# Performance work log

Hardware: AMD Instinct MI355X
Metric: run time of the kernel (lower is better)

Reference implementation:

```python
import jax, jax.numpy as jnp
import numpy as np
import math

THETA = 10000.0

def apply_rope(x):
    # x: [B, H, S, D] with D even; interleaved even/odd rotation
    B, H, S, D = x.shape
    dim_half = D // 2
    freq_idx = jnp.arange(dim_half, dtype=jnp.float32)
    inv_freq = jnp.exp(-math.log(THETA) * freq_idx * 2.0 / D)  # [D/2]
    pos = jnp.arange(S, dtype=jnp.float32)
    angles = pos[:, None] * inv_freq[None, :]      # [S, D/2]
    cos = jnp.cos(angles)[None, None]              # [1,1,S,D/2]
    sin = jnp.sin(angles)[None, None]
    x_even = x[..., ::2]
    x_odd = x[..., 1::2]
    r_even = x_even * cos - x_odd * sin
    r_odd = x_odd * cos + x_even * sin
    return jnp.stack([r_even, r_odd], axis=-1).reshape(B, H, S, D)

def setup_inputs() -> dict:
    key = jax.random.key(0)
    ks = jax.random.split(key, 5)
    B, S, E = 2, 2048, 1024
    std = 0.02
    inp = {
        "hidden_states": jax.random.normal(ks[0], (B, S, E), dtype=jnp.float32),
        "Wq": jax.random.normal(ks[1], (E, E), dtype=jnp.float32) * std,
        "bq": jnp.zeros((E,), dtype=jnp.float32),
        "Wk": jax.random.normal(ks[2], (E, E), dtype=jnp.float32) * std,
        "bk": jnp.zeros((E,), dtype=jnp.float32),
        "Wv": jax.random.normal(ks[3], (E, E), dtype=jnp.float32) * std,
        "bv": jnp.zeros((E,), dtype=jnp.float32),
        "Wo": jax.random.normal(ks[4], (E, E), dtype=jnp.float32) * std,
        "bo": jnp.zeros((E,), dtype=jnp.float32),
    }
    return inp

def reference(hidden_states, Wq, bq, Wk, bk, Wv, bv, Wo, bo):
    NUM_HEADS = 16
    B, S, E = hidden_states.shape
    D = E // NUM_HEADS
    scale = 1.0 / math.sqrt(D)

    def proj(W, b):
        # torch Linear: x @ W.T + b; then [B,S,H,D] -> [B,H,S,D]
        y = hidden_states @ W.T + b
        return y.reshape(B, S, NUM_HEADS, D).transpose(0, 2, 1, 3)

    q = apply_rope(proj(Wq, bq))
    k = apply_rope(proj(Wk, bk))
    v = proj(Wv, bv)

    scores = jnp.einsum("bhqd,bhkd->bhqk", q, k) * scale
    attn = jax.nn.softmax(scores, axis=-1)
    out = jnp.einsum("bhqk,bhkd->bhqd", attn, v)  # [B,H,S,D]
    out = out.transpose(0, 2, 1, 3).reshape(B, S, E)
    return out @ Wo.T + bo  # dropout: eval mode (identity)
```

## Files before the change

kernel.cpp:

```cpp
#include <hip/hip_runtime.h>
#include <hip/hip_bf16.h>
#include <math.h>

#define B_ 2
#define S_ 2048
#define E_ 1024
#define H_ 16
#define D_ 64
#define M_ (B_*S_)
#define PT 32

typedef short bf16x8 __attribute__((ext_vector_type(8)));
typedef float f32x4 __attribute__((ext_vector_type(4)));
typedef unsigned short u16x4 __attribute__((ext_vector_type(4)));

#define SCLQ 0.18033688011112042f

__device__ __forceinline__ unsigned short f2bf(float f) {
    unsigned int u = __builtin_bit_cast(unsigned int, f);
    u += 0x7FFFu + ((u >> 16) & 1u);
    return (unsigned short)(u >> 16);
}
__device__ __forceinline__ unsigned int pk2bf(float a, float b) {
    __hip_bfloat162 h = __float22bfloat162_rn(make_float2(a, b));
    unsigned int u;
    __builtin_memcpy(&u, &h, 4);
    return u;
}
__device__ __forceinline__ f32x4 mfma16(bf16x8 a, bf16x8 b, f32x4 c) {
    return __builtin_amdgcn_mfma_f32_16x16x32_bf16(a, b, c, 0, 0, 0);
}
__device__ __forceinline__ bf16x8 cvt8(const float* p) {
    f32x4 lo = *(const f32x4*)p;
    f32x4 hi = *(const f32x4*)(p + 4);
    unsigned int pk[4];
    pk[0] = pk2bf(lo[0], lo[1]);
    pk[1] = pk2bf(lo[2], lo[3]);
    pk[2] = pk2bf(hi[0], hi[1]);
    pk[3] = pk2bf(hi[2], hi[3]);
    bf16x8 r;
    __builtin_memcpy(&r, pk, 16);
    return r;
}
__device__ __forceinline__ void g2l16(const unsigned short* g, unsigned short* l) {
    __builtin_amdgcn_global_load_lds(
        (const __attribute__((address_space(1))) unsigned int*)(const void*)g,
        (__attribute__((address_space(3))) unsigned int*)(void*)l,
        16, 0, 0);
}

__global__ __launch_bounds__(256) void cvt_kernel(
    const float* __restrict__ X,  const float* __restrict__ Wq,
    const float* __restrict__ Wk, const float* __restrict__ Wv,
    const float* __restrict__ Wo,
    unsigned short* __restrict__ Xb, unsigned short* __restrict__ Wb,
    float* __restrict__ tab)
{
    const int y = blockIdx.y;
    if (y == 5) {
        unsigned int i = blockIdx.x * 256 + threadIdx.x;
        if (i < 32 * 2048) {
            int f = i >> 11, s = i & 2047;
            const float C = -0.41524101186091903f;
            const float INV2PI = 0.15915494309189535f;
            float inv_rev = exp2f(C * (float)f) * INV2PI;
            float rev = (float)s * inv_rev;
            float fr = rev - rintf(rev);
            tab[i]           = __builtin_amdgcn_cosf(fr);
            tab[65536 + i]   = __builtin_amdgcn_sinf(fr);
        }
        return;
    }
    const float* src = (y == 0) ? X : (y == 1) ? Wq : (y == 2) ? Wk : (y == 3) ? Wv : Wo;
    unsigned short* dst = (y == 0) ? Xb : Wb + (size_t)(y - 1) * (E_ * E_);
    const size_t n = (y == 0) ? (size_t)M_ * E_ : (size_t)E_ * E_;
    size_t i = ((size_t)blockIdx.x * 256 + threadIdx.x) * 8;
    if (i < n) *(bf16x8*)(dst + i) = cvt8(src + i);
}

__global__ __launch_bounds__(256, 4) void qkv_rope_bf(
    const unsigned short* __restrict__ Xb, const unsigned short* __restrict__ Wb,
    const float* __restrict__ bq, const float* __restrict__ bk,
    const float* __restrict__ bv, const float* __restrict__ tab,
    unsigned short* __restrict__ Qo, unsigned short* __restrict__ Ko,
    unsigned short* __restrict__ Vo)
{
    __shared__ __align__(16) unsigned char lds_raw[128 * 132 * 2];
    unsigned short* As = (unsigned short*)lds_raw;
    unsigned short* Bs = (unsigned short*)(lds_raw + 8192);
    unsigned short* Cs = (unsigned short*)lds_raw;

    const int t = threadIdx.x;
    const int w = t >> 6, lane = t & 63, quad = lane >> 4, l16 = lane & 15;
    const int wr = (w >> 1) * 64, wc = (w & 1) * 64;
    const int n0 = blockIdx.x * 128, m0 = blockIdx.y * 128;
    const int z = blockIdx.z;
    const unsigned short* W = Wb + (size_t)z * (E_ * E_);
    const float* bias = (z == 0) ? bq : (z == 1) ? bk : bv;

    const int r4 = t >> 2, c8 = (t & 3) * 8;
    const unsigned short* Ag = Xb + (size_t)(m0 + r4) * E_ + c8;
    const unsigned short* Bg = W  + (size_t)(n0 + r4) * E_ + c8;

    f32x4 zero = {0.f, 0.f, 0.f, 0.f};
    f32x4 acc[4][4];
#pragma unroll
    for (int i = 0; i < 4; i++)
#pragma unroll
        for (int j = 0; j < 4; j++) acc[i][j] = zero;

    for (int kt = 0; kt < E_; kt += 32) {
        __syncthreads();
        g2l16(Ag + kt,           &As[t * 8]);
        g2l16(Ag + 64 * E_ + kt, &As[t * 8 + 2048]);
        g2l16(Bg + kt,           &Bs[t * 8]);
        g2l16(Bg + 64 * E_ + kt, &Bs[t * 8 + 2048]);
        __syncthreads();
        bf16x8 af[4], bfr[4];
#pragma unroll
        for (int i = 0; i < 4; i++)
            af[i] = *(const bf16x8*)&As[(wr + i * 16 + l16) * 32 + quad * 8];
#pragma unroll
        for (int j = 0; j < 4; j++)
            bfr[j] = *(const bf16x8*)&Bs[(wc + j * 16 + l16) * 32 + quad * 8];
#pragma unroll
        for (int i = 0; i < 4; i++)
#pragma unroll
            for (int j = 0; j < 4; j++)
                acc[i][j] = mfma16(af[i], bfr[j], acc[i][j]);
    }

    __syncthreads();
    const int seg = quad;
    if (z < 2) {
        const float qscale = (z == 0) ? SCLQ : 1.0f;
#pragma unroll
        for (int j = 0; j < 4; j++) {
            int n_local = wc + j * 16 + l16;
            int n = n0 + n_local;
            int d = n & 63, f = d >> 1;
            float bvv = bias[n];
            float sgn = (d & 1) ? 1.f : -1.f;
            const float* ct = tab + f * 2048;
            const float* st_ = tab + 65536 + f * 2048;
#pragma unroll
            for (int i = 0; i < 4; i++) {
                int mb = wr + i * 16 + quad * 4;
                int sb = (m0 + mb) & (S_ - 1);
                f32x4 cs4 = *(const f32x4*)&ct[sb];
                f32x4 sn4 = *(const f32x4*)&st_[sb];
#pragma unroll
                for (int r = 0; r < 4; r++) {
                    float val = acc[i][j][r] + bvv;
                    float oth = __shfl_xor(val, 1);
                    Cs[(mb + r) * 132 + n_local] =
                        f2bf((val * cs4[r] + sgn * oth * sn4[r]) * qscale);
                }
            }
        }
        __syncthreads();
        unsigned short* Out = (z == 0) ? Qo : Ko;
        const int btok = m0 >> 11;
        const int half = seg & 1;
#pragma unroll
        for (int it = 0; it < 16; it++) {
            int m_local = it * 8 + w * 2 + (seg >> 1);
            int s = (m0 + m_local) & (S_ - 1);
            int h = (n0 + half * 64) >> 6;
            u16x4 v = *(const u16x4*)&Cs[m_local * 132 + half * 64 + l16 * 4];
            *(u16x4*)&Out[(((size_t)btok * H_ + h) * S_ + s) * D_ + l16 * 4] = v;
        }
    } else {
#pragma unroll
        for (int j = 0; j < 4; j++) {
            int n_local = wc + j * 16 + l16;
            float bvv = bias[n0 + n_local];
#pragma unroll
            for (int i = 0; i < 4; i++) {
                int mb = wr + i * 16 + quad * 4;
#pragma unroll
                for (int r = 0; r < 4; r++)
                    Cs[n_local * 132 + mb + r] = f2bf(acc[i][j][r] + bvv);
            }
        }
        __syncthreads();
        const int btok = m0 >> 11;
        const int s0 = m0 & (S_ - 1);
        const int half = seg & 1;
#pragma unroll
        for (int it = 0; it < 16; it++) {
            int n_local = it * 8 + w * 2 + (seg >> 1);
            int n = n0 + n_local;
            int h = n >> 6, d = n & 63;
            u16x4 v = *(const u16x4*)&Cs[n_local * 132 + half * 64 + l16 * 4];
            *(u16x4*)&Vo[(((size_t)btok * H_ + h) * D_ + d) * S_ + s0 + half * 64 + l16 * 4] = v;
        }
    }
}

__global__ __launch_bounds__(512, 3) void attn_direct(
    const unsigned short* __restrict__ Q, const unsigned short* __restrict__ K,
    const unsigned short* __restrict__ Vt, unsigned short* __restrict__ ctx)
{
    __shared__ unsigned short KsD[2][64 * 64];
    __shared__ unsigned short VsD[2][64 * 64];
    __shared__ unsigned short Ps[8][16 * 72];
    const int t = threadIdx.x;
    const int w = t >> 6, lane = t & 63, quad = lane >> 4, l16 = lane & 15;
    const int bh = blockIdx.y;
    const int q0 = blockIdx.x * 128 + w * 16;

    const unsigned short* Qg = Q + ((size_t)bh * S_ + q0) * D_;
    bf16x8 qf[2];
#pragma unroll
    for (int ks = 0; ks < 2; ks++)
        qf[ks] = *(const bf16x8*)(Qg + (size_t)l16 * 64 + ks * 32 + quad * 8);

    bf16x8 ones;
#pragma unroll
    for (int e = 0; e < 8; e++) ones[e] = (short)0x3F80;

    f32x4 zero = {0.f, 0.f, 0.f, 0.f};
    f32x4 acc_o[4];
    f32x4 acc_l = zero;
#pragma unroll
    for (int j = 0; j < 4; j++) acc_o[j] = zero;

    const int tt = t & 255, ksel = t >> 8;
    const int sr = tt >> 2;
    const int sc = ((tt & 3) ^ ((tt >> 3) & 3)) * 8;
    const unsigned short* KgL = K  + (size_t)bh * S_ * D_ + (size_t)sr * 64 + ksel * 32 + sc;
    const unsigned short* VgL = Vt + (size_t)bh * D_ * S_ + (size_t)sr * S_ + ksel * 32 + sc;

    const int sl = (quad ^ ((l16 >> 1) & 3)) * 8;

    g2l16(KgL, &KsD[0][t * 8]);
    g2l16(VgL, &VsD[0][t * 8]);
    __syncthreads();

    int p = 0;
    for (int kt = 0; kt < S_; kt += 64) {
        if (kt + 64 < S_) {
            g2l16(KgL + (size_t)(kt + 64) * 64, &KsD[1 - p][t * 8]);
            g2l16(VgL + (kt + 64),              &VsD[1 - p][t * 8]);
        }

        f32x4 sc4[4];
#pragma unroll
        for (int j = 0; j < 4; j++) sc4[j] = zero;
#pragma unroll
        for (int ks = 0; ks < 2; ks++) {
#pragma unroll
            for (int j = 0; j < 4; j++) {
                bf16x8 kf = *(const bf16x8*)&KsD[p][ks * 2048 + (j * 16 + l16) * 32 + sl];
                sc4[j] = mfma16(qf[ks], kf, sc4[j]);
            }
        }
#pragma unroll
        for (int j = 0; j < 4; j++)
#pragma unroll
            for (int r = 0; r < 4; r += 2) {
                float pa = __builtin_amdgcn_exp2f(sc4[j][r]);
                float pb = __builtin_amdgcn_exp2f(sc4[j][r + 1]);
                unsigned int u = pk2bf(pa, pb);
                Ps[w][(quad * 4 + r)     * 72 + j * 16 + l16] = (unsigned short)u;
                Ps[w][(quad * 4 + r + 1) * 72 + j * 16 + l16] = (unsigned short)(u >> 16);
            }
#pragma unroll
        for (int ks = 0; ks < 2; ks++) {
            bf16x8 pf = *(const bf16x8*)&Ps[w][l16 * 72 + ks * 32 + quad * 8];
#pragma unroll
            for (int jd = 0; jd < 4; jd++) {
                bf16x8 vf = *(const bf16x8*)&VsD[p][ks * 2048 + (jd * 16 + l16) * 32 + sl];
                acc_o[jd] = mfma16(pf, vf, acc_o[jd]);
            }
            acc_l = mfma16(pf, ones, acc_l);
        }

        __syncthreads();
        p ^= 1;
    }

    const int b = bh >> 4, h = bh & 15;
    f32x4 rl;
#pragma unroll
    for (int r = 0; r < 4; r++) rl[r] = 1.0f / acc_l[r];
#pragma unroll
    for (int jd = 0; jd < 4; jd++)
#pragma unroll
        for (int r = 0; r < 4; r++) {
            int qrow = q0 + quad * 4 + r;
            int col = h * 64 + jd * 16 + l16;
            ctx[((size_t)b * S_ + qrow) * E_ + col] = f2bf(acc_o[jd][r] * rl[r]);
        }
}

__global__ __launch_bounds__(256, 4) void out_bf(
    const unsigned short* __restrict__ Cx, const unsigned short* __restrict__ Wob,
    const float* __restrict__ bo, float* __restrict__ out)
{
    __shared__ unsigned short As[128 * 32];
    __shared__ unsigned short Bs[64 * 32];
    const int t = threadIdx.x;
    const int w = t >> 6, lane = t & 63, quad = lane >> 4, l16 = lane & 15;
    const int m0 = blockIdx.y * 128, n0 = blockIdx.x * 64;
    const int wr = w * 32;
    const int r4 = t >> 2, c8 = (t & 3) * 8;
    const unsigned short* Ag = Cx  + (size_t)(m0 + r4) * E_ + c8;
    const unsigned short* Bg = Wob + (size_t)(n0 + r4) * E_ + c8;

    f32x4 zero = {0.f, 0.f, 0.f, 0.f};
    f32x4 acc[2][4];
#pragma unroll
    for (int i = 0; i < 2; i++)
#pragma unroll
        for (int j = 0; j < 4; j++) acc[i][j] = zero;

    for (int kt = 0; kt < E_; kt += 32) {
        __syncthreads();
        g2l16(Ag + kt,           &As[t * 8]);
        g2l16(Ag + 64 * E_ + kt, &As[t * 8 + 2048]);
        g2l16(Bg + kt,           &Bs[t * 8]);
        __syncthreads();
        bf16x8 af[2], bfr[4];
#pragma unroll
        for (int i = 0; i < 2; i++)
            af[i] = *(const bf16x8*)&As[(wr + i * 16 + l16) * 32 + quad * 8];
#pragma unroll
        for (int j = 0; j < 4; j++)
            bfr[j] = *(const bf16x8*)&Bs[(j * 16 + l16) * 32 + quad * 8];
#pragma unroll
        for (int i = 0; i < 2; i++)
#pragma unroll
            for (int j = 0; j < 4; j++)
                acc[i][j] = mfma16(af[i], bfr[j], acc[i][j]);
    }

#pragma unroll
    for (int j = 0; j < 4; j++) {
        int n = n0 + j * 16 + l16;
        float bvv = bo[n];
#pragma unroll
        for (int i = 0; i < 2; i++) {
            int mrow = m0 + wr + i * 16 + quad * 4;
#pragma unroll
            for (int r = 0; r < 4; r++)
                out[(size_t)(mrow + r) * E_ + n] = acc[i][j][r] + bvv;
        }
    }
}

__global__ __launch_bounds__(256, 3) void qkv_rope_f32(
    const float* __restrict__ X,
    const float* __restrict__ Wq, const float* __restrict__ Wk,
    const float* __restrict__ Wv,
    const float* __restrict__ bq, const float* __restrict__ bk,
    const float* __restrict__ bv,
    unsigned short* __restrict__ Qo, unsigned short* __restrict__ Ko,
    unsigned short* __restrict__ Vo)
{
    __shared__ __align__(16) unsigned char lds_raw[128 * 132 * 2];
    unsigned short* As = (unsigned short*)lds_raw;
    unsigned short* Bs = (unsigned short*)(lds_raw + 8192);
    unsigned short* Cs = (unsigned short*)lds_raw;

    const int t = threadIdx.x;
    const int w = t >> 6, lane = t & 63, quad = lane >> 4, l16 = lane & 15;
    const int wr = (w >> 1) * 64, wc = (w & 1) * 64;
    const int n0 = blockIdx.x * 128, m0 = blockIdx.y * 128;
    const int z = blockIdx.z;
    const float* W    = (z == 0) ? Wq : (z == 1) ? Wk : Wv;
    const float* bias = (z == 0) ? bq : (z == 1) ? bk : bv;

    const int r4 = t >> 2, c8 = (t & 3) * 8;
    const int st = r4 * PT + c8;
    const float* Ag = X + (size_t)(m0 + r4) * E_ + c8;
    const float* Bg = W + (size_t)(n0 + r4) * E_ + c8;

    f32x4 zero = {0.f, 0.f, 0.f, 0.f};
    f32x4 acc[4][4];
#pragma unroll
    for (int i = 0; i < 4; i++)
#pragma unroll
        for (int j = 0; j < 4; j++) acc[i][j] = zero;

    for (int kt = 0; kt < E_; kt += 32) {
        bf16x8 a0 = cvt8(Ag + kt);
        bf16x8 a1 = cvt8(Ag + 64 * E_ + kt);
        bf16x8 b0 = cvt8(Bg + kt);
        bf16x8 b1 = cvt8(Bg + 64 * E_ + kt);
        __syncthreads();
        *(bf16x8*)&As[st]           = a0;
        *(bf16x8*)&As[st + 64 * PT] = a1;
        *(bf16x8*)&Bs[st]           = b0;
        *(bf16x8*)&Bs[st + 64 * PT] = b1;
        __syncthreads();
        bf16x8 af[4], bfr[4];
#pragma unroll
        for (int i = 0; i < 4; i++)
            af[i] = *(const bf16x8*)&As[(wr + i * 16 + l16) * PT + quad * 8];
#pragma unroll
        for (int j = 0; j < 4; j++)
            bfr[j] = *(const bf16x8*)&Bs[(wc + j * 16 + l16) * PT + quad * 8];
#pragma unroll
        for (int i = 0; i < 4; i++)
#pragma unroll
            for (int j = 0; j < 4; j++)
                acc[i][j] = mfma16(af[i], bfr[j], acc[i][j]);
    }

    __syncthreads();
    const int seg = quad;
    if (z < 2) {
        const float C = -0.41524101186091903f;
        const float INV2PI = 0.15915494309189535f;
        const float qscale = (z == 0) ? SCLQ : 1.0f;
#pragma unroll
        for (int j = 0; j < 4; j++) {
            int n_local = wc + j * 16 + l16;
            int n = n0 + n_local;
            int d = n & 63, f = d >> 1;
            float inv_rev = exp2f(C * (float)f) * INV2PI;
            float bvv = bias[n];
            float sgn = (d & 1) ? 1.f : -1.f;
#pragma unroll
            for (int i = 0; i < 4; i++) {
                int mb = wr + i * 16 + quad * 4;
#pragma unroll
                for (int r = 0; r < 4; r++) {
                    int m = m0 + mb + r;
                    int s = m & (S_ - 1);
                    float val = acc[i][j][r] + bvv;
                    float oth = __shfl_xor(val, 1);
                    float rev = (float)s * inv_rev;
                    float fr = rev - rintf(rev);
                    float sn = __builtin_amdgcn_sinf(fr);
                    float cs = __builtin_amdgcn_cosf(fr);
                    Cs[(mb + r) * 132 + n_local] =
                        f2bf((val * cs + sgn * oth * sn) * qscale);
                }
            }
        }
        __syncthreads();
        unsigned short* Out = (z == 0) ? Qo : Ko;
        const int btok = m0 >> 11;
        const int half = seg & 1;
#pragma unroll
        for (int it = 0; it < 16; it++) {
            int m_local = it * 8 + w * 2 + (seg >> 1);
            int s = (m0 + m_local) & (S_ - 1);
            int h = (n0 + half * 64) >> 6;
            u16x4 v = *(const u16x4*)&Cs[m_local * 132 + half * 64 + l16 * 4];
            *(u16x4*)&Out[(((size_t)btok * H_ + h) * S_ + s) * D_ + l16 * 4] = v;
        }
    } else {
#pragma unroll
        for (int j = 0; j < 4; j++) {
            int n_local = wc + j * 16 + l16;
            float bvv = bias[n0 + n_local];
#pragma unroll
            for (int i = 0; i < 4; i++) {
                int mb = wr + i * 16 + quad * 4;
#pragma unroll
                for (int r = 0; r < 4; r++)
                    Cs[n_local * 132 + mb + r] = f2bf(acc[i][j][r] + bvv);
            }
        }
        __syncthreads();
        const int btok = m0 >> 11;
        const int s0 = m0 & (S_ - 1);
        const int half = seg & 1;
#pragma unroll
        for (int it = 0; it < 16; it++) {
            int n_local = it * 8 + w * 2 + (seg >> 1);
            int n = n0 + n_local;
            int h = n >> 6, d = n & 63;
            u16x4 v = *(const u16x4*)&Cs[n_local * 132 + half * 64 + l16 * 4];
            *(u16x4*)&Vo[(((size_t)btok * H_ + h) * D_ + d) * S_ + s0 + half * 64 + l16 * 4] = v;
        }
    }
}

__global__ __launch_bounds__(256, 2) void out_f32(
    const unsigned short* __restrict__ Cx, const float* __restrict__ Wo,
    const float* __restrict__ bo, float* __restrict__ out)
{
    __shared__ unsigned short As[128 * PT];
    __shared__ unsigned short Bs[64 * PT];
    const int t = threadIdx.x;
    const int w = t >> 6, lane = t & 63, quad = lane >> 4, l16 = lane & 15;
    const int m0 = blockIdx.y * 128, n0 = blockIdx.x * 64;
    const int wr = w * 32;
    const int r4 = t >> 2, c8 = (t & 3) * 8;
    const int st = r4 * PT + c8;
    const unsigned short* Ag = Cx + (size_t)(m0 + r4) * E_ + c8;
    const float*          Bg = Wo + (size_t)(n0 + (r4 & 63)) * E_ + c8;

    f32x4 zero = {0.f, 0.f, 0.f, 0.f};
    f32x4 acc[2][4];
#pragma unroll
    for (int i = 0; i < 2; i++)
#pragma unroll
        for (int j = 0; j < 4; j++) acc[i][j] = zero;

    for (int kt = 0; kt < E_; kt += 32) {
        bf16x8 a0 = *(const bf16x8*)(Ag + kt);
        bf16x8 a1 = *(const bf16x8*)(Ag + 64 * E_ + kt);
        bf16x8 b0 = cvt8(Bg + kt);
        __syncthreads();
        *(bf16x8*)&As[st]           = a0;
        *(bf16x8*)&As[st + 64 * PT] = a1;
        *(bf16x8*)&Bs[st]           = b0;
        __syncthreads();
        bf16x8 af[2], bfr[4];
#pragma unroll
        for (int i = 0; i < 2; i++)
            af[i] = *(const bf16x8*)&As[(wr + i * 16 + l16) * PT + quad * 8];
#pragma unroll
        for (int j = 0; j < 4; j++)
            bfr[j] = *(const bf16x8*)&Bs[(j * 16 + l16) * PT + quad * 8];
#pragma unroll
        for (int i = 0; i < 2; i++)
#pragma unroll
            for (int j = 0; j < 4; j++)
                acc[i][j] = mfma16(af[i], bfr[j], acc[i][j]);
    }

#pragma unroll
    for (int j = 0; j < 4; j++) {
        int n = n0 + j * 16 + l16;
        float bvv = bo[n];
#pragma unroll
        for (int i = 0; i < 2; i++) {
            int mrow = m0 + wr + i * 16 + quad * 4;
#pragma unroll
            for (int r = 0; r < 4; r++)
                out[(size_t)(mrow + r) * E_ + n] = acc[i][j][r] + bvv;
        }
    }
}

extern "C" void kernel_launch(void* const* d_in, const int* in_sizes, int n_in,
                              void* d_out, int out_size, void* d_ws, size_t ws_size,
                              hipStream_t stream) {
    const float* X  = (const float*)d_in[0];
    const float* Wq = (const float*)d_in[1];
    const float* bq = (const float*)d_in[2];
    const float* Wk = (const float*)d_in[3];
    const float* bk = (const float*)d_in[4];
    const float* Wv = (const float*)d_in[5];
    const float* bv = (const float*)d_in[6];
    const float* Wo = (const float*)d_in[7];
    const float* bo = (const float*)d_in[8];
    float* outp = (float*)d_out;

    const size_t TN = (size_t)B_ * H_ * S_ * D_;
    const size_t need_f32 = 4 * TN * sizeof(unsigned short);
    const size_t need_bf  = 5 * TN * sizeof(unsigned short) + 2 * 65536 * sizeof(float);
    if (ws_size < need_f32) return;

    unsigned short* Qb = (unsigned short*)d_ws;
    unsigned short* Kb = Qb + TN;
    unsigned short* Vb = Kb + TN;

    if (ws_size >= need_bf) {
        unsigned short* Xb = Vb + TN;
        unsigned short* Wb = Xb + TN;
        float* tab = (float*)(Wb + 4 * (size_t)(E_ * E_));
        unsigned short* Cx = Xb;

        cvt_kernel<<<dim3(2048, 6), 256, 0, stream>>>(X, Wq, Wk, Wv, Wo, Xb, Wb, tab);
        qkv_rope_bf<<<dim3(E_ / 128, M_ / 128, 3), 256, 0, stream>>>(
            Xb, Wb, bq, bk, bv, tab, Qb, Kb, Vb);
        attn_direct<<<dim3(S_ / 128, B_ * H_), 512, 0, stream>>>(Qb, Kb, Vb, Cx);
        out_bf<<<dim3(E_ / 64, M_ / 128), 256, 0, stream>>>(
            Cx, Wb + 3 * (size_t)(E_ * E_), bo, outp);
    } else {
        unsigned short* Cx = Vb + TN;
        qkv_rope_f32<<<dim3(E_ / 128, M_ / 128, 3), 256, 0, stream>>>(
            X, Wq, Wk, Wv, bq, bk, bv, Qb, Kb, Vb);
        attn_direct<<<dim3(S_ / 128, B_ * H_), 512, 0, stream>>>(Qb, Kb, Vb, Cx);
        out_f32<<<dim3(E_ / 64, M_ / 128), 256, 0, stream>>>(Cx, Wo, bo, outp);
    }
}
```

Measured before the change: 196.8 us.

## Software-pipeline attention: overlap next QK^T with current PV using triple-buffered K/V

```diff
diff --git a/kernel.cpp b/kernel.cpp
--- a/kernel.cpp
+++ b/kernel.cpp
@@ -198,17 +198,18 @@
     }
 }
 
-__global__ __launch_bounds__(512, 3) void attn_direct(
+__global__ __launch_bounds__(512, 2) void attn_direct(
     const unsigned short* __restrict__ Q, const unsigned short* __restrict__ K,
     const unsigned short* __restrict__ Vt, unsigned short* __restrict__ ctx)
 {
-    __shared__ unsigned short KsD[2][64 * 64];
-    __shared__ unsigned short VsD[2][64 * 64];
+    __shared__ unsigned short Ks[3][64 * 64];
+    __shared__ unsigned short Vs[3][64 * 64];
     __shared__ unsigned short Ps[8][16 * 72];
     const int t = threadIdx.x;
     const int w = t >> 6, lane = t & 63, quad = lane >> 4, l16 = lane & 15;
     const int bh = blockIdx.y;
     const int q0 = blockIdx.x * 128 + w * 16;
+    const int NT = S_ / 64;
 
     const unsigned short* Qg = Q + ((size_t)bh * S_ + q0) * D_;
     bf16x8 qf[2];
@@ -234,28 +235,22 @@
 
     const int sl = (quad ^ ((l16 >> 1) & 3)) * 8;
 
-    g2l16(KgL, &KsD[0][t * 8]);
-    g2l16(VgL, &VsD[0][t * 8]);
+    g2l16(KgL, &Ks[0][t * 8]);
+    g2l16(VgL, &Vs[0][t * 8]);
     __syncthreads();
-
-    int p = 0;
-    for (int kt = 0; kt < S_; kt += 64) {
-        if (kt + 64 < S_) {
-            g2l16(KgL + (size_t)(kt + 64) * 64, &KsD[1 - p][t * 8]);
-            g2l16(VgL + (kt + 64),              &VsD[1 - p][t * 8]);
-        }
-
+    g2l16(KgL + 4096, &Ks[1][t * 8]);
+    g2l16(VgL + 64,   &Vs[1][t * 8]);
+    {
         f32x4 sc4[4];
 #pragma unroll
         for (int j = 0; j < 4; j++) sc4[j] = zero;
 #pragma unroll
-        for (int ks = 0; ks < 2; ks++) {
+        for (int ks = 0; ks < 2; ks++)
 #pragma unroll
             for (int j = 0; j < 4; j++) {
-                bf16x8 kf = *(const bf16x8*)&KsD[p][ks * 2048 + (j * 16 + l16) * 32 + sl];
+                bf16x8 kf = *(const bf16x8*)&Ks[0][ks * 2048 + (j * 16 + l16) * 32 + sl];
                 sc4[j] = mfma16(qf[ks], kf, sc4[j]);
             }
-        }
 #pragma unroll
         for (int j = 0; j < 4; j++)
 #pragma unroll
@@ -266,19 +261,72 @@
                 Ps[w][(quad * 4 + r)     * 72 + j * 16 + l16] = (unsigned short)u;
                 Ps[w][(quad * 4 + r + 1) * 72 + j * 16 + l16] = (unsigned short)(u >> 16);
             }
-#pragma unroll
-        for (int ks = 0; ks < 2; ks++) {
-            bf16x8 pf = *(const bf16x8*)&Ps[w][l16 * 72 + ks * 32 + quad * 8];
-#pragma unroll
-            for (int jd = 0; jd < 4; jd++) {
-                bf16x8 vf = *(const bf16x8*)&VsD[p][ks * 2048 + (jd * 16 + l16) * 32 + sl];
-                acc_o[jd] = mfma16(pf, vf, acc_o[jd]);
-            }
-            acc_l = mfma16(pf, ones, acc_l);
-        }
-
-        __syncthreads();
-        p ^= 1;
+    }
+
+    int bc = 0, bn = 1, bx = 2;
+    for (int i = 0; i < NT - 1; ++i) {
+        __syncthreads();
+        if (i + 2 < NT) {
+            g2l16(KgL + (size_t)(i + 2) * 4096, &Ks[bx][t * 8]);
+            g2l16(VgL + (i + 2) * 64,           &Vs[bx][t * 8]);
+        }
+        bf16x8 pf0 = *(const bf16x8*)&Ps[w][l16 * 72 + quad * 8];
+        bf16x8 pf1 = *(const bf16x8*)&Ps[w][l16 * 72 + 32 + quad * 8];
+
+        __builtin_amdgcn_s_setprio(1);
+        f32x4 scn[4];
+#pragma unroll
+        for (int j = 0; j < 4; j++) scn[j] = zero;
+#pragma unroll
+        for (int ks = 0; ks < 2; ks++)
+#pragma unroll
+            for (int j = 0; j < 4; j++) {
+                bf16x8 kf = *(const bf16x8*)&Ks[bn][ks * 2048 + (j * 16 + l16) * 32 + sl];
+                scn[j] = mfma16(qf[ks], kf, scn[j]);
+            }
+#pragma unroll
+        for (int jd = 0; jd < 4; jd++) {
+            bf16x8 vf = *(const bf16x8*)&Vs[bc][(jd * 16 + l16) * 32 + sl];
+            acc_o[jd] = mfma16(pf0, vf, acc_o[jd]);
+        }
+        acc_l = mfma16(pf0, ones, acc_l);
+#pragma unroll
+        for (int jd = 0; jd < 4; jd++) {
+            bf16x8 vf = *(const bf16x8*)&Vs[bc][2048 + (jd * 16 + l16) * 32 + sl];
+            acc_o[jd] = mfma16(pf1, vf, acc_o[jd]);
+        }
+        acc_l = mfma16(pf1, ones, acc_l);
+        __builtin_amdgcn_s_setprio(0);
+
+#pragma unroll
+        for (int j = 0; j < 4; j++)
+#pragma unroll
+            for (int r = 0; r < 4; r += 2) {
+                float pa = __builtin_amdgcn_exp2f(scn[j][r]);
+                float pb = __builtin_amdgcn_exp2f(scn[j][r + 1]);
+                unsigned int u = pk2bf(pa, pb);
+                Ps[w][(quad * 4 + r)     * 72 + j * 16 + l16] = (unsigned short)u;
+                Ps[w][(quad * 4 + r + 1) * 72 + j * 16 + l16] = (unsigned short)(u >> 16);
+            }
+
+        int tb = bc; bc = bn; bn = bx; bx = tb;
+    }
+
+    {
+        bf16x8 pf0 = *(const bf16x8*)&Ps[w][l16 * 72 + quad * 8];
+        bf16x8 pf1 = *(const bf16x8*)&Ps[w][l16 * 72 + 32 + quad * 8];
+#pragma unroll
+        for (int jd = 0; jd < 4; jd++) {
+            bf16x8 vf = *(const bf16x8*)&Vs[bc][(jd * 16 + l16) * 32 + sl];
+            acc_o[jd] = mfma16(pf0, vf, acc_o[jd]);
+        }
+        acc_l = mfma16(pf0, ones, acc_l);
+#pragma unroll
+        for (int jd = 0; jd < 4; jd++) {
+            bf16x8 vf = *(const bf16x8*)&Vs[bc][2048 + (jd * 16 + l16) * 32 + sl];
+            acc_o[jd] = mfma16(pf1, vf, acc_o[jd]);
+        }
+        acc_l = mfma16(pf1, ones, acc_l);
     }
 
     const int b = bh >> 4, h = bh & 15;
```

New measurement: 191.7 us. 1.03x faster.
